# Kernel optimization log

Measured on AMD Instinct MI355X. Metric: run time of the kernel, lower is better.

Reference implementation:

```python
import math
import jax, jax.numpy as jnp
import numpy as np

B, T, C, H = 4, 2048, 1024, 16
D = C // H  # head dim = 64


def setup_inputs() -> dict:
    key = jax.random.key(0)
    ks = jax.random.split(key, 9)
    s = 1.0 / math.sqrt(C)
    return {
        "x": jax.random.normal(ks[0], (B, T, C), jnp.float32),
        "Wq": jax.random.normal(ks[1], (C, C), jnp.float32) * s,
        "bq": jax.random.normal(ks[2], (C,), jnp.float32) * 0.02,
        "Wk": jax.random.normal(ks[3], (C, C), jnp.float32) * s,
        "bk": jax.random.normal(ks[4], (C,), jnp.float32) * 0.02,
        "Wv": jax.random.normal(ks[5], (C, C), jnp.float32) * s,
        "bv": jax.random.normal(ks[6], (C,), jnp.float32) * 0.02,
        "Wo": jax.random.normal(ks[7], (C, C), jnp.float32) * s,
        "bo": jax.random.normal(ks[8], (C,), jnp.float32) * 0.02,
    }


def reference(x, Wq, bq, Wk, bk, Wv, bv, Wo, bo):
    # Projections: (B,T,C) -> (B,H,T,D)
    def heads(y):
        return y.reshape(B, T, H, D).transpose(0, 2, 1, 3)

    q = heads(x @ Wq + bq)
    k = heads(x @ Wk + bk)
    v = heads(x @ Wv + bv)

    scale = 1.0 / math.sqrt(D)
    scores = jnp.einsum("bhqd,bhkd->bhqk", q, k) * scale  # (B,H,T,T)
    causal = jnp.tril(jnp.ones((T, T), dtype=bool))
    scores = jnp.where(causal[None, None], scores, jnp.float32(-jnp.inf))
    att = jax.nn.softmax(scores, axis=-1)

    y = jnp.einsum("bhqk,bhkd->bhqd", att, v)  # (B,H,T,D)
    y = y.transpose(0, 2, 1, 3).reshape(B, T, C)
    return y @ Wo + bo
```

## Files before the change

### kernel.cpp

```cpp
#include <hip/hip_runtime.h>

#define B_ 4
#define T_ 2048
#define C_ 1024
#define H_ 16
#define D_ 64
#define M_ (B_*T_)

typedef unsigned short u16;
typedef __attribute__((ext_vector_type(8))) short short8;
typedef __attribute__((ext_vector_type(8))) unsigned short ushort8_t;
typedef __attribute__((ext_vector_type(4))) unsigned short ushort4_t;
typedef __attribute__((ext_vector_type(4))) float floatx4;
typedef __attribute__((ext_vector_type(16))) float f32x16;
typedef __attribute__((ext_vector_type(4))) unsigned int uint4_t;

__device__ __forceinline__ u16 f2bf(float f) {
  union { float f; unsigned u; } v; v.f = f;
  unsigned r = v.u + 0x7fffu + ((v.u >> 16) & 1u);
  return (u16)(r >> 16);
}

__device__ __forceinline__ void gload16(const void* g, void* l) {
  __builtin_amdgcn_global_load_lds((__attribute__((address_space(1))) void*)(g),
                                   (__attribute__((address_space(3))) void*)(l),
                                   16, 0, 0);
}

__device__ __forceinline__ unsigned cvtpk(float lo, float hi) {
  unsigned r;
  asm("v_cvt_pk_bf16_f32 %0, %1, %2" : "=v"(r) : "v"(lo), "v"(hi));
  return r;
}

__device__ __forceinline__ void pl32swap(unsigned &a, unsigned &b) {
  asm volatile("v_permlane32_swap_b32 %0, %1" : "+v"(a), "+v"(b));
}

__global__ __launch_bounds__(256) void convx_k(const float* __restrict__ x,
                                               u16* __restrict__ o) {
  int i = (blockIdx.x * 256 + threadIdx.x) * 4;
  floatx4 v = *(const floatx4*)(x + i);
  ushort4_t r;
#pragma unroll
  for (int j = 0; j < 4; ++j) r[j] = f2bf(v[j]);
  *(ushort4_t*)(o + i) = r;
}

__global__ __launch_bounds__(256) void wconv_k(const float* __restrict__ W0,
                                               const float* __restrict__ W1,
                                               const float* __restrict__ W2,
                                               const float* __restrict__ W3,
                                               u16* __restrict__ WT) {
  __shared__ float tile[64][65];
  const float* W = blockIdx.z == 0 ? W0 : blockIdx.z == 1 ? W1 : blockIdx.z == 2 ? W2 : W3;
  u16* Wt = WT + (size_t)blockIdx.z * (C_ * C_);
  int k0 = blockIdx.x * 64, n0 = blockIdx.y * 64;
  int t = threadIdx.x;
  int r = t >> 2, c0 = (t & 3) * 16;
#pragma unroll
  for (int j = 0; j < 4; ++j) {
    floatx4 v = *(const floatx4*)(W + (size_t)(k0 + r) * C_ + n0 + c0 + j * 4);
#pragma unroll
    for (int jj = 0; jj < 4; ++jj) tile[r][c0 + j * 4 + jj] = v[jj];
  }
  __syncthreads();
  ushort8_t o0, o1;
#pragma unroll
  for (int j = 0; j < 8; ++j) o0[j] = f2bf(tile[c0 + j][r]);
#pragma unroll
  for (int j = 0; j < 8; ++j) o1[j] = f2bf(tile[c0 + 8 + j][r]);
  *(ushort8_t*)(Wt + (size_t)(n0 + r) * C_ + k0 + c0) = o0;
  *(ushort8_t*)(Wt + (size_t)(n0 + r) * C_ + k0 + c0 + 8) = o1;
}

template <int OUTF32>
__global__ __launch_bounds__(256, 2) void gemm_k(const u16* __restrict__ A,
                                                 const u16* __restrict__ Wt,
                                                 const float* __restrict__ bias,
                                                 void* __restrict__ Cout, float scale) {
  __shared__ u16 As[128 * 32];
  __shared__ u16 Bs[128 * 32];
  const int tid = threadIdx.x;
  const int w = tid >> 6, lane = tid & 63;
  const int wr = (w >> 1) * 64, wc = (w & 1) * 64;
  const int l15 = lane & 15, g = lane >> 4;
  const int m0 = blockIdx.x * 128, n0 = blockIdx.y * 128;

  floatx4 acc[4][4] = {};

  const u16* ga = A + (size_t)(m0 + (tid >> 2)) * C_ + (tid & 3) * 8;
  const u16* gb = Wt + (size_t)(n0 + (tid >> 2)) * C_ + (tid & 3) * 8;
  u16* lA = As + tid * 8;
  u16* lB = Bs + tid * 8;

  for (int kt = 0; kt < C_; kt += 32) {
    gload16(ga + kt, lA);
    gload16(ga + kt + (size_t)64 * C_, lA + 64 * 32);
    gload16(gb + kt, lB);
    gload16(gb + kt + (size_t)64 * C_, lB + 64 * 32);
    asm volatile("s_waitcnt vmcnt(0)" ::: "memory");
    __syncthreads();
    short8 af[4], bf[4];
#pragma unroll
    for (int i = 0; i < 4; ++i)
      af[i] = *(const short8*)(As + (wr + i * 16 + l15) * 32 + g * 8);
#pragma unroll
    for (int i = 0; i < 4; ++i)
      bf[i] = *(const short8*)(Bs + (wc + i * 16 + l15) * 32 + g * 8);
#pragma unroll
    for (int mi = 0; mi < 4; ++mi)
#pragma unroll
      for (int ni = 0; ni < 4; ++ni)
        acc[mi][ni] = __builtin_amdgcn_mfma_f32_16x16x32_bf16(af[mi], bf[ni], acc[mi][ni], 0, 0, 0);
    __syncthreads();
  }
#pragma unroll
  for (int mi = 0; mi < 4; ++mi) {
    int row = m0 + wr + mi * 16 + g * 4;
#pragma unroll
    for (int ni = 0; ni < 4; ++ni) {
      int col = n0 + wc + ni * 16 + l15;
      float bv = bias[col];
#pragma unroll
      for (int i = 0; i < 4; ++i) {
        float v = (acc[mi][ni][i] + bv) * scale;
        if (OUTF32)
          ((float*)Cout)[(size_t)(row + i) * C_ + col] = v;
        else
          ((u16*)Cout)[(size_t)(row + i) * C_ + col] = f2bf(v);
      }
    }
  }
}

__global__ __launch_bounds__(512, 2) void attn_k(const u16* __restrict__ Qg,
                                                 const u16* __restrict__ Kg,
                                                 const u16* __restrict__ Vg,
                                                 u16* __restrict__ Yg) {
  __shared__ u16 Ks[2][64 * 64];
  __shared__ u16 Vt[2][64 * 64];

  const int tid = threadIdx.x;
  const int w = tid >> 6, lane = tid & 63;
  const int qi = lane & 31, h = lane >> 5;

  const int lid = blockIdx.x + 8 * blockIdx.y;
  const int xcd = lid & 7, slot = lid >> 3;
  const int bxl = 7 - (slot >> 3);
  const int bh = xcd + 8 * (slot & 7);
  const int q0 = bxl * 256;
  const size_t base = (size_t)(bh >> 4) * ((size_t)T_ * C_) + (size_t)(bh & 15) * D_;
  const int qw0 = q0 + w * 32;
  const int q_abs = qw0 + qi;

  const int srow = tid >> 3, schunk = tid & 7;
  const int sgcol = (schunk ^ (srow & 7)) * 8;
  const u16* Kgr = Kg + base + (size_t)srow * C_ + sgcol;
  const u16* Vgr = Vg + base + (size_t)srow * C_ + schunk * 8;

  short8 qf[4];
  {
    const u16* Qr = Qg + base + (size_t)q_abs * C_ + 8 * h;
#pragma unroll
    for (int c = 0; c < 4; ++c) qf[c] = *(const short8*)(Qr + 16 * c);
  }

  gload16(Kgr, &Ks[0][tid * 8]);
  ushort8_t va = *(const ushort8_t*)(Vgr);

  f32x16 y0 = {}, y1 = {};
  float m_run = -3e38f, l_run = 0.f;
  const int nt = 4 * bxl + 4;

  for (int t = 0; t < nt; ++t) {
    u16* Kb = Ks[t & 1];
    u16* Vb = Vt[t & 1];
    asm volatile("s_waitcnt vmcnt(0)" ::: "memory");
#pragma unroll
    for (int j = 0; j < 8; ++j) {
      int d = schunk * 8 + j;
      *(u16*)((char*)Vb + d * 128 + ((2 * srow) ^ (j << 4))) = va[j];
    }
    __syncthreads();
    if (t + 1 < nt) {
      gload16(Kgr + (size_t)(t + 1) * 64 * C_, &Ks[(t + 1) & 1][tid * 8]);
      va = *(const ushort8_t*)(Vgr + (size_t)(t + 1) * 64 * C_);
    }

    const int kv0 = t * 64;
    if (kv0 <= qw0 + 31) {
      f32x16 s0 = {}, s1 = {};
      {
        const char* kbase = (const char*)Kb;
        const int sw = (qi & 7) << 4;
        const char* kr0 = kbase + qi * 128;
        const char* kr1 = kbase + (qi + 32) * 128;
#pragma unroll
        for (int c = 0; c < 4; ++c) {
          int col = (32 * c + 16 * h) ^ sw;
          short8 k0 = *(const short8*)(kr0 + col);
          short8 k1 = *(const short8*)(kr1 + col);
          s0 = __builtin_amdgcn_mfma_f32_32x32x16_bf16(k0, qf[c], s0, 0, 0, 0);
          s1 = __builtin_amdgcn_mfma_f32_32x32x16_bf16(k1, qf[c], s1, 0, 0, 0);
        }
      }
      if (kv0 + 63 > qw0) {
#pragma unroll
        for (int r = 0; r < 16; ++r) {
          int kvq = (r & 3) + 8 * (r >> 2) + 4 * h;
          if (kv0 + kvq > q_abs) s0[r] = -1e30f;
          if (kv0 + 32 + kvq > q_abs) s1[r] = -1e30f;
        }
      }
      float pm = s0[0];
#pragma unroll
      for (int r = 1; r < 16; ++r) pm = fmaxf(pm, s0[r]);
#pragma unroll
      for (int r = 0; r < 16; ++r) pm = fmaxf(pm, s1[r]);
      pm = fmaxf(pm, __shfl_xor(pm, 32));
      if (!__all(pm <= m_run + 8.0f)) {
        float mnew = fmaxf(m_run, pm);
        float corr = __builtin_amdgcn_exp2f(m_run - mnew);
        m_run = mnew;
        l_run *= corr;
#pragma unroll
        for (int r = 0; r < 16; ++r) {
          float cq = __shfl(corr, (r & 3) + 8 * (r >> 2) + 4 * h);
          y0[r] *= cq;
          y1[r] *= cq;
        }
      }
      float rs = 0.f;
#pragma unroll
      for (int r = 0; r < 16; ++r) { s0[r] = __builtin_amdgcn_exp2f(s0[r] - m_run); rs += s0[r]; }
#pragma unroll
      for (int r = 0; r < 16; ++r) { s1[r] = __builtin_amdgcn_exp2f(s1[r] - m_run); rs += s1[r]; }
      rs += __shfl_xor(rs, 32);
      l_run += rs;

      float pv[32];
#pragma unroll
      for (int r = 0; r < 16; ++r) { pv[r] = s0[r]; pv[16 + r] = s1[r]; }
      unsigned pw[16];
#pragma unroll
      for (int c = 0; c < 4; ++c) {
        const int rb = c * 8;
        unsigned a0 = cvtpk(pv[rb + 0], pv[rb + 1]);
        unsigned b0 = cvtpk(pv[rb + 4], pv[rb + 5]);
        pl32swap(a0, b0);
        unsigned a1 = cvtpk(pv[rb + 2], pv[rb + 3]);
        unsigned b1 = cvtpk(pv[rb + 6], pv[rb + 7]);
        pl32swap(a1, b1);
        pw[c * 4 + 0] = a0; pw[c * 4 + 1] = a1;
        pw[c * 4 + 2] = b0; pw[c * 4 + 3] = b1;
      }
      {
        const char* vb0 = (const char*)Vb + qi * 128;
        const char* vb1 = (const char*)Vb + (qi + 32) * 128;
        const int swd = (qi & 7) << 4;
#pragma unroll
        for (int c = 0; c < 4; ++c) {
          int col = (32 * c + 16 * h) ^ swd;
          uint4_t pt = {pw[c * 4 + 0], pw[c * 4 + 1], pw[c * 4 + 2], pw[c * 4 + 3]};
          short8 pa = __builtin_bit_cast(short8, pt);
          short8 v0 = *(const short8*)(vb0 + col);
          short8 v1 = *(const short8*)(vb1 + col);
          y0 = __builtin_amdgcn_mfma_f32_32x32x16_bf16(pa, v0, y0, 0, 0, 0);
          y1 = __builtin_amdgcn_mfma_f32_32x32x16_bf16(pa, v1, y1, 0, 0, 0);
        }
      }
    }
    __syncthreads();
  }

  float linv = 1.0f / l_run;
#pragma unroll
  for (int r = 0; r < 16; ++r) {
    int qp = (r & 3) + 8 * (r >> 2) + 4 * h;
    float lv = __shfl(linv, qp);
    size_t row = base + (size_t)(qw0 + qp) * C_;
    Yg[row + qi] = f2bf(y0[r] * lv);
    Yg[row + 32 + qi] = f2bf(y1[r] * lv);
  }
}

extern "C" void kernel_launch(void* const* d_in, const int* in_sizes, int n_in,
                              void* d_out, int out_size, void* d_ws, size_t ws_size,
                              hipStream_t stream) {
  const float* x  = (const float*)d_in[0];
  const float* Wq = (const float*)d_in[1];
  const float* bq = (const float*)d_in[2];
  const float* Wk = (const float*)d_in[3];
  const float* bk = (const float*)d_in[4];
  const float* Wv = (const float*)d_in[5];
  const float* bv = (const float*)d_in[6];
  const float* Wo = (const float*)d_in[7];
  const float* bo = (const float*)d_in[8];
  float* out = (float*)d_out;

  char* ws = (char*)d_ws;
  u16* xb = (u16*)ws;
  u16* WT = (u16*)(ws + (size_t)16777216);
  u16* Qb = (u16*)(ws + (size_t)25165824);
  u16* Kb = (u16*)(ws + (size_t)41943040);
  u16* Vb = (u16*)(ws + (size_t)58720256);
  u16* Yb = xb;

  convx_k<<<dim3(M_ * C_ / 1024), 256, 0, stream>>>(x, xb);
  wconv_k<<<dim3(16, 16, 4), 256, 0, stream>>>(Wq, Wk, Wv, Wo, WT);
  gemm_k<0><<<dim3(64, 8), 256, 0, stream>>>(xb, WT + (size_t)0 * 1048576, bq, Qb, 0.125f * 1.44269504f);
  gemm_k<0><<<dim3(64, 8), 256, 0, stream>>>(xb, WT + (size_t)1 * 1048576, bk, Kb, 1.0f);
  gemm_k<0><<<dim3(64, 8), 256, 0, stream>>>(xb, WT + (size_t)2 * 1048576, bv, Vb, 1.0f);
  attn_k<<<dim3(8, 64), 512, 0, stream>>>(Qb, Kb, Vb, Yb);
  gemm_k<1><<<dim3(64, 8), 256, 0, stream>>>(Yb, WT + (size_t)3 * 1048576, bo, out, 1.0f);
}
```

Before: 197.7 us.

## Fuse QKV projections into one GEMM and pair causal query tiles in attention

Folds the softmax scale into the converted Wq weights and merges the three Q/K/V projection GEMMs into a single launch writing an interleaved QKV buffer with a 3072 stride. The attention kernel moves to 256-thread blocks with 1D indexing, and each block handles two 128-row query tiles (j and 15-j), so every block does the same amount of causal work. The goal is fewer launches, better wave fill in the projection, and less tail imbalance in attention. In exchange, Q is now scaled before rounding to bf16 rather than after, the epilogue picks a bias by segment, and the attention loop is longer and heavy on macros, with more live Q registers.

```diff
diff --git a/kernel.cpp b/kernel.cpp
--- a/kernel.cpp
+++ b/kernel.cpp
@@ -6,6 +6,7 @@
 #define H_ 16
 #define D_ 64
 #define M_ (B_*T_)
+#define CR3 3072
 
 typedef unsigned short u16;
 typedef __attribute__((ext_vector_type(8))) short short8;
@@ -37,6 +38,8 @@
   asm volatile("v_permlane32_swap_b32 %0, %1" : "+v"(a), "+v"(b));
 }
 
+#define MFMA32(a, b, c) __builtin_amdgcn_mfma_f32_32x32x16_bf16(a, b, c, 0, 0, 0)
+
 __global__ __launch_bounds__(256) void convx_k(const float* __restrict__ x,
                                                u16* __restrict__ o) {
   int i = (blockIdx.x * 256 + threadIdx.x) * 4;
@@ -54,6 +57,7 @@
                                                u16* __restrict__ WT) {
   __shared__ float tile[64][65];
   const float* W = blockIdx.z == 0 ? W0 : blockIdx.z == 1 ? W1 : blockIdx.z == 2 ? W2 : W3;
+  const float sc = blockIdx.z == 0 ? 0.125f * 1.44269504f : 1.0f;
   u16* Wt = WT + (size_t)blockIdx.z * (C_ * C_);
   int k0 = blockIdx.x * 64, n0 = blockIdx.y * 64;
   int t = threadIdx.x;
@@ -67,9 +71,9 @@
   __syncthreads();
   ushort8_t o0, o1;
 #pragma unroll
-  for (int j = 0; j < 8; ++j) o0[j] = f2bf(tile[c0 + j][r]);
-#pragma unroll
-  for (int j = 0; j < 8; ++j) o1[j] = f2bf(tile[c0 + 8 + j][r]);
+  for (int j = 0; j < 8; ++j) o0[j] = f2bf(tile[c0 + j][r] * sc);
+#pragma unroll
+  for (int j = 0; j < 8; ++j) o1[j] = f2bf(tile[c0 + 8 + j][r] * sc);
   *(ushort8_t*)(Wt + (size_t)(n0 + r) * C_ + k0 + c0) = o0;
   *(ushort8_t*)(Wt + (size_t)(n0 + r) * C_ + k0 + c0 + 8) = o1;
 }
@@ -77,8 +81,11 @@
 template <int OUTF32>
 __global__ __launch_bounds__(256, 2) void gemm_k(const u16* __restrict__ A,
                                                  const u16* __restrict__ Wt,
-                                                 const float* __restrict__ bias,
-                                                 void* __restrict__ Cout, float scale) {
+                                                 const float* __restrict__ b0,
+                                                 const float* __restrict__ b1,
+                                                 const float* __restrict__ b2,
+                                                 float bsc0,
+                                                 void* __restrict__ Cout, int ostride) {
   __shared__ u16 As[128 * 32];
   __shared__ u16 Bs[128 * 32];
   const int tid = threadIdx.x;
@@ -121,22 +128,22 @@
 #pragma unroll
     for (int ni = 0; ni < 4; ++ni) {
       int col = n0 + wc + ni * 16 + l15;
-      float bv = bias[col];
+      int seg = col >> 10;
+      const float* bp = seg == 0 ? b0 : seg == 1 ? b1 : b2;
+      float bv = bp[col & 1023] * (seg == 0 ? bsc0 : 1.0f);
 #pragma unroll
       for (int i = 0; i < 4; ++i) {
-        float v = (acc[mi][ni][i] + bv) * scale;
+        float v = acc[mi][ni][i] + bv;
         if (OUTF32)
-          ((float*)Cout)[(size_t)(row + i) * C_ + col] = v;
+          ((float*)Cout)[(size_t)(row + i) * ostride + col] = v;
         else
-          ((u16*)Cout)[(size_t)(row + i) * C_ + col] = f2bf(v);
+          ((u16*)Cout)[(size_t)(row + i) * ostride + col] = f2bf(v);
       }
     }
   }
 }
 
-__global__ __launch_bounds__(512, 2) void attn_k(const u16* __restrict__ Qg,
-                                                 const u16* __restrict__ Kg,
-                                                 const u16* __restrict__ Vg,
+__global__ __launch_bounds__(256, 2) void attn_k(const u16* __restrict__ QKV,
                                                  u16* __restrict__ Yg) {
   __shared__ u16 Ks[2][64 * 64];
   __shared__ u16 Vt[2][64 * 64];
@@ -145,143 +152,175 @@
   const int w = tid >> 6, lane = tid & 63;
   const int qi = lane & 31, h = lane >> 5;
 
-  const int lid = blockIdx.x + 8 * blockIdx.y;
-  const int xcd = lid & 7, slot = lid >> 3;
-  const int bxl = 7 - (slot >> 3);
-  const int bh = xcd + 8 * (slot & 7);
-  const int q0 = bxl * 256;
-  const size_t base = (size_t)(bh >> 4) * ((size_t)T_ * C_) + (size_t)(bh & 15) * D_;
-  const int qw0 = q0 + w * 32;
-  const int q_abs = qw0 + qi;
+  const int lid = blockIdx.x;
+  const int xcd = lid & 7, t2 = lid >> 3;
+  const int bh = xcd + 8 * (t2 & 7);
+  const int p = t2 >> 3;
+  const int jA = p, jB = 15 - p;
+  const int nA = 2 * jA + 2;
+
+  const size_t baseQ = (size_t)(bh >> 4) * T_ * CR3 + (size_t)(bh & 15) * D_;
+  const size_t baseY = (size_t)(bh >> 4) * T_ * C_ + (size_t)(bh & 15) * D_;
+  const u16* Kg = QKV + baseQ + 1024;
+  const u16* Vg = QKV + baseQ + 2048;
 
   const int srow = tid >> 3, schunk = tid & 7;
   const int sgcol = (schunk ^ (srow & 7)) * 8;
-  const u16* Kgr = Kg + base + (size_t)srow * C_ + sgcol;
-  const u16* Vgr = Vg + base + (size_t)srow * C_ + schunk * 8;
-
-  short8 qf[4];
+  const u16* Kgr = Kg + (size_t)srow * CR3 + sgcol;
+  const u16* Vgr = Vg + (size_t)srow * CR3 + schunk * 8;
+
+  short8 qA0, qA1, qA2, qA3, qB0, qB1, qB2, qB3;
   {
-    const u16* Qr = Qg + base + (size_t)q_abs * C_ + 8 * h;
-#pragma unroll
-    for (int c = 0; c < 4; ++c) qf[c] = *(const short8*)(Qr + 16 * c);
-  }
-
+    const u16* Qa = QKV + baseQ + (size_t)(128 * jA + 32 * w + qi) * CR3 + 8 * h;
+    const u16* Qb = QKV + baseQ + (size_t)(128 * jB + 32 * w + qi) * CR3 + 8 * h;
+    qA0 = *(const short8*)(Qa);      qA1 = *(const short8*)(Qa + 16);
+    qA2 = *(const short8*)(Qa + 32); qA3 = *(const short8*)(Qa + 48);
+    qB0 = *(const short8*)(Qb);      qB1 = *(const short8*)(Qb + 16);
+    qB2 = *(const short8*)(Qb + 32); qB3 = *(const short8*)(Qb + 48);
+  }
+
+  ushort8_t va, vbr;
   gload16(Kgr, &Ks[0][tid * 8]);
-  ushort8_t va = *(const ushort8_t*)(Vgr);
+  gload16(Kgr + (size_t)32 * CR3, &Ks[0][2048 + tid * 8]);
+  va = *(const ushort8_t*)(Vgr);
+  vbr = *(const ushort8_t*)(Vgr + (size_t)32 * CR3);
 
   f32x16 y0 = {}, y1 = {};
   float m_run = -3e38f, l_run = 0.f;
-  const int nt = 4 * bxl + 4;
-
-  for (int t = 0; t < nt; ++t) {
-    u16* Kb = Ks[t & 1];
-    u16* Vb = Vt[t & 1];
-    asm volatile("s_waitcnt vmcnt(0)" ::: "memory");
-#pragma unroll
-    for (int j = 0; j < 8; ++j) {
-      int d = schunk * 8 + j;
-      *(u16*)((char*)Vb + d * 128 + ((2 * srow) ^ (j << 4))) = va[j];
+
+#define PREFETCH(IT2) do { \
+    if ((IT2) < 34) { \
+      int nkv_ = ((IT2) >= nA ? (IT2) - nA : (IT2)) * 64; \
+      u16* dst_ = Ks[(IT2) & 1]; \
+      gload16(Kgr + (size_t)nkv_ * CR3, dst_ + tid * 8); \
+      gload16(Kgr + (size_t)(nkv_ + 32) * CR3, dst_ + 2048 + tid * 8); \
+      va = *(const ushort8_t*)(Vgr + (size_t)nkv_ * CR3); \
+      vbr = *(const ushort8_t*)(Vgr + (size_t)(nkv_ + 32) * CR3); \
+    } } while (0)
+
+#define SCATTERV(VB) do { \
+    char* vbp_ = (char*)(VB); \
+    _Pragma("unroll") for (int j = 0; j < 8; ++j) { \
+      int d_ = schunk * 8 + j; \
+      *(u16*)(vbp_ + d_ * 128 + ((2 * srow) ^ (j << 4))) = va[j]; \
+      *(u16*)(vbp_ + d_ * 128 + ((2 * (srow + 32)) ^ (j << 4))) = vbr[j]; \
+    } } while (0)
+
+#define COMPUTE(KB, VB, KV0, QW0, QF0, QF1, QF2, QF3) do { \
+    const int q_abs_ = (QW0) + qi; \
+    f32x16 s0 = {}, s1 = {}; \
+    { const int swq_ = (qi & 7) << 4; \
+      const char* kr0_ = (const char*)(KB) + qi * 128; \
+      const char* kr1_ = (const char*)(KB) + (qi + 32) * 128; \
+      short8 k0_, k1_; \
+      k0_ = *(const short8*)(kr0_ + ((16 * h) ^ swq_)); \
+      k1_ = *(const short8*)(kr1_ + ((16 * h) ^ swq_)); \
+      s0 = MFMA32(k0_, QF0, s0); s1 = MFMA32(k1_, QF0, s1); \
+      k0_ = *(const short8*)(kr0_ + ((32 + 16 * h) ^ swq_)); \
+      k1_ = *(const short8*)(kr1_ + ((32 + 16 * h) ^ swq_)); \
+      s0 = MFMA32(k0_, QF1, s0); s1 = MFMA32(k1_, QF1, s1); \
+      k0_ = *(const short8*)(kr0_ + ((64 + 16 * h) ^ swq_)); \
+      k1_ = *(const short8*)(kr1_ + ((64 + 16 * h) ^ swq_)); \
+      s0 = MFMA32(k0_, QF2, s0); s1 = MFMA32(k1_, QF2, s1); \
+      k0_ = *(const short8*)(kr0_ + ((96 + 16 * h) ^ swq_)); \
+      k1_ = *(const short8*)(kr1_ + ((96 + 16 * h) ^ swq_)); \
+      s0 = MFMA32(k0_, QF3, s0); s1 = MFMA32(k1_, QF3, s1); \
+    } \
+    if ((KV0) + 63 > (QW0)) { \
+      _Pragma("unroll") for (int r = 0; r < 16; ++r) { \
+        int kvq_ = (r & 3) + 8 * (r >> 2) + 4 * h; \
+        if ((KV0) + kvq_ > q_abs_) s0[r] = -1e30f; \
+        if ((KV0) + 32 + kvq_ > q_abs_) s1[r] = -1e30f; \
+      } \
+    } \
+    float pm_ = s0[0]; \
+    _Pragma("unroll") for (int r = 1; r < 16; ++r) pm_ = fmaxf(pm_, s0[r]); \
+    _Pragma("unroll") for (int r = 0; r < 16; ++r) pm_ = fmaxf(pm_, s1[r]); \
+    pm_ = fmaxf(pm_, __shfl_xor(pm_, 32)); \
+    if (!__all(pm_ <= m_run + 8.0f)) { \
+      float mnew_ = fmaxf(m_run, pm_); \
+      float corr_ = __builtin_amdgcn_exp2f(m_run - mnew_); \
+      m_run = mnew_; \
+      l_run *= corr_; \
+      _Pragma("unroll") for (int r = 0; r < 16; ++r) { \
+        float cq_ = __shfl(corr_, (r & 3) + 8 * (r >> 2) + 4 * h); \
+        y0[r] *= cq_; y1[r] *= cq_; \
+      } \
+    } \
+    float rs_ = 0.f; \
+    _Pragma("unroll") for (int r = 0; r < 16; ++r) { s0[r] = __builtin_amdgcn_exp2f(s0[r] - m_run); rs_ += s0[r]; } \
+    _Pragma("unroll") for (int r = 0; r < 16; ++r) { s1[r] = __builtin_amdgcn_exp2f(s1[r] - m_run); rs_ += s1[r]; } \
+    rs_ += __shfl_xor(rs_, 32); \
+    l_run += rs_; \
+    float pv_[32]; \
+    _Pragma("unroll") for (int r = 0; r < 16; ++r) { pv_[r] = s0[r]; pv_[16 + r] = s1[r]; } \
+    unsigned pw_[16]; \
+    _Pragma("unroll") for (int c = 0; c < 4; ++c) { \
+      const int rb_ = c * 8; \
+      unsigned a0_ = cvtpk(pv_[rb_ + 0], pv_[rb_ + 1]); \
+      unsigned b0_ = cvtpk(pv_[rb_ + 4], pv_[rb_ + 5]); \
+      pl32swap(a0_, b0_); \
+      unsigned a1_ = cvtpk(pv_[rb_ + 2], pv_[rb_ + 3]); \
+      unsigned b1_ = cvtpk(pv_[rb_ + 6], pv_[rb_ + 7]); \
+      pl32swap(a1_, b1_); \
+      pw_[c * 4 + 0] = a0_; pw_[c * 4 + 1] = a1_; \
+      pw_[c * 4 + 2] = b0_; pw_[c * 4 + 3] = b1_; \
+    } \
+    { const char* vb0_ = (const char*)(VB) + qi * 128; \
+      const char* vb1_ = (const char*)(VB) + (qi + 32) * 128; \
+      const int swd_ = (qi & 7) << 4; \
+      _Pragma("unroll") for (int c = 0; c < 4; ++c) { \
+        int col_ = (32 * c + 16 * h) ^ swd_; \
+        uint4_t pt_ = {pw_[c * 4 + 0], pw_[c * 4 + 1], pw_[c * 4 + 2], pw_[c * 4 + 3]}; \
+        short8 pa_ = __builtin_bit_cast(short8, pt_); \
+        short8 v0_ = *(const short8*)(vb0_ + col_); \
+        short8 v1_ = *(const short8*)(vb1_ + col_); \
+        y0 = MFMA32(pa_, v0_, y0); \
+        y1 = MFMA32(pa_, v1_, y1); \
+      } \
+    } } while (0)
+
+#define STOREY(J) do { \
+    float linv_ = 1.0f / l_run; \
+    _Pragma("unroll") for (int r = 0; r < 16; ++r) { \
+      int qp_ = (r & 3) + 8 * (r >> 2) + 4 * h; \
+      float lv_ = __shfl(linv_, qp_); \
+      size_t row_ = baseY + (size_t)(128 * (J) + 32 * w + qp_) * C_; \
+      Yg[row_ + qi] = f2bf(y0[r] * lv_); \
+      Yg[row_ + 32 + qi] = f2bf(y1[r] * lv_); \
+    } } while (0)
+
+  {
+    const int qw0 = 128 * jA + 32 * w;
+    for (int it = 0; it < nA; ++it) {
+      const int kv0 = it * 64;
+      u16* Kb = Ks[it & 1];
+      u16* Vb = Vt[it & 1];
+      asm volatile("s_waitcnt vmcnt(0)" ::: "memory");
+      SCATTERV(Vb);
+      __syncthreads();
+      PREFETCH(it + 1);
+      if (kv0 <= qw0 + 31) COMPUTE(Kb, Vb, kv0, qw0, qA0, qA1, qA2, qA3);
+      __syncthreads();
     }
-    __syncthreads();
-    if (t + 1 < nt) {
-      gload16(Kgr + (size_t)(t + 1) * 64 * C_, &Ks[(t + 1) & 1][tid * 8]);
-      va = *(const ushort8_t*)(Vgr + (size_t)(t + 1) * 64 * C_);
+    STOREY(jA);
+  }
+  y0 = (f32x16){}; y1 = (f32x16){};
+  m_run = -3e38f; l_run = 0.f;
+  {
+    const int qw0 = 128 * jB + 32 * w;
+    for (int it = nA; it < 34; ++it) {
+      const int kv0 = (it - nA) * 64;
+      u16* Kb = Ks[it & 1];
+      u16* Vb = Vt[it & 1];
+      asm volatile("s_waitcnt vmcnt(0)" ::: "memory");
+      SCATTERV(Vb);
+      __syncthreads();
+      PREFETCH(it + 1);
+      if (kv0 <= qw0 + 31) COMPUTE(Kb, Vb, kv0, qw0, qB0, qB1, qB2, qB3);
+      __syncthreads();
     }
-
-    const int kv0 = t * 64;
-    if (kv0 <= qw0 + 31) {
-      f32x16 s0 = {}, s1 = {};
-      {
-        const char* kbase = (const char*)Kb;
-        const int sw = (qi & 7) << 4;
-        const char* kr0 = kbase + qi * 128;
-        const char* kr1 = kbase + (qi + 32) * 128;
-#pragma unroll
-        for (int c = 0; c < 4; ++c) {
-          int col = (32 * c + 16 * h) ^ sw;
-          short8 k0 = *(const short8*)(kr0 + col);
-          short8 k1 = *(const short8*)(kr1 + col);
-          s0 = __builtin_amdgcn_mfma_f32_32x32x16_bf16(k0, qf[c], s0, 0, 0, 0);
-          s1 = __builtin_amdgcn_mfma_f32_32x32x16_bf16(k1, qf[c], s1, 0, 0, 0);
-        }
-      }
-      if (kv0 + 63 > qw0) {
-#pragma unroll
-        for (int r = 0; r < 16; ++r) {
-          int kvq = (r & 3) + 8 * (r >> 2) + 4 * h;
-          if (kv0 + kvq > q_abs) s0[r] = -1e30f;
-          if (kv0 + 32 + kvq > q_abs) s1[r] = -1e30f;
-        }
-      }
-      float pm = s0[0];
-#pragma unroll
-      for (int r = 1; r < 16; ++r) pm = fmaxf(pm, s0[r]);
-#pragma unroll
-      for (int r = 0; r < 16; ++r) pm = fmaxf(pm, s1[r]);
-      pm = fmaxf(pm, __shfl_xor(pm, 32));
-      if (!__all(pm <= m_run + 8.0f)) {
-        float mnew = fmaxf(m_run, pm);
-        float corr = __builtin_amdgcn_exp2f(m_run - mnew);
-        m_run = mnew;
-        l_run *= corr;
-#pragma unroll
-        for (int r = 0; r < 16; ++r) {
-          float cq = __shfl(corr, (r & 3) + 8 * (r >> 2) + 4 * h);
-          y0[r] *= cq;
-          y1[r] *= cq;
-        }
-      }
-      float rs = 0.f;
-#pragma unroll
-      for (int r = 0; r < 16; ++r) { s0[r] = __builtin_amdgcn_exp2f(s0[r] - m_run); rs += s0[r]; }
-#pragma unroll
-      for (int r = 0; r < 16; ++r) { s1[r] = __builtin_amdgcn_exp2f(s1[r] - m_run); rs += s1[r]; }
-      rs += __shfl_xor(rs, 32);
-      l_run += rs;
-
-      float pv[32];
-#pragma unroll
-      for (int r = 0; r < 16; ++r) { pv[r] = s0[r]; pv[16 + r] = s1[r]; }
-      unsigned pw[16];
-#pragma unroll
-      for (int c = 0; c < 4; ++c) {
-        const int rb = c * 8;
-        unsigned a0 = cvtpk(pv[rb + 0], pv[rb + 1]);
-        unsigned b0 = cvtpk(pv[rb + 4], pv[rb + 5]);
-        pl32swap(a0, b0);
-        unsigned a1 = cvtpk(pv[rb + 2], pv[rb + 3]);
-        unsigned b1 = cvtpk(pv[rb + 6], pv[rb + 7]);
-        pl32swap(a1, b1);
-        pw[c * 4 + 0] = a0; pw[c * 4 + 1] = a1;
-        pw[c * 4 + 2] = b0; pw[c * 4 + 3] = b1;
-      }
-      {
-        const char* vb0 = (const char*)Vb + qi * 128;
-        const char* vb1 = (const char*)Vb + (qi + 32) * 128;
-        const int swd = (qi & 7) << 4;
-#pragma unroll
-        for (int c = 0; c < 4; ++c) {
-          int col = (32 * c + 16 * h) ^ swd;
-          uint4_t pt = {pw[c * 4 + 0], pw[c * 4 + 1], pw[c * 4 + 2], pw[c * 4 + 3]};
-          short8 pa = __builtin_bit_cast(short8, pt);
-          short8 v0 = *(const short8*)(vb0 + col);
-          short8 v1 = *(const short8*)(vb1 + col);
-          y0 = __builtin_amdgcn_mfma_f32_32x32x16_bf16(pa, v0, y0, 0, 0, 0);
-          y1 = __builtin_amdgcn_mfma_f32_32x32x16_bf16(pa, v1, y1, 0, 0, 0);
-        }
-      }
-    }
-    __syncthreads();
-  }
-
-  float linv = 1.0f / l_run;
-#pragma unroll
-  for (int r = 0; r < 16; ++r) {
-    int qp = (r & 3) + 8 * (r >> 2) + 4 * h;
-    float lv = __shfl(linv, qp);
-    size_t row = base + (size_t)(qw0 + qp) * C_;
-    Yg[row + qi] = f2bf(y0[r] * lv);
-    Yg[row + 32 + qi] = f2bf(y1[r] * lv);
+    STOREY(jB);
   }
 }
 
@@ -300,18 +339,16 @@
   float* out = (float*)d_out;
 
   char* ws = (char*)d_ws;
-  u16* xb = (u16*)ws;
-  u16* WT = (u16*)(ws + (size_t)16777216);
-  u16* Qb = (u16*)(ws + (size_t)25165824);
-  u16* Kb = (u16*)(ws + (size_t)41943040);
-  u16* Vb = (u16*)(ws + (size_t)58720256);
+  u16* xb   = (u16*)ws;
+  u16* WT   = (u16*)(ws + (size_t)16777216);
+  u16* QKVb = (u16*)(ws + (size_t)25165824);
   u16* Yb = xb;
 
   convx_k<<<dim3(M_ * C_ / 1024), 256, 0, stream>>>(x, xb);
   wconv_k<<<dim3(16, 16, 4), 256, 0, stream>>>(Wq, Wk, Wv, Wo, WT);
-  gemm_k<0><<<dim3(64, 8), 256, 0, stream>>>(xb, WT + (size_t)0 * 1048576, bq, Qb, 0.125f * 1.44269504f);
-  gemm_k<0><<<dim3(64, 8), 256, 0, stream>>>(xb, WT + (size_t)1 * 1048576, bk, Kb, 1.0f);
-  gemm_k<0><<<dim3(64, 8), 256, 0, stream>>>(xb, WT + (size_t)2 * 1048576, bv, Vb, 1.0f);
-  attn_k<<<dim3(8, 64), 512, 0, stream>>>(Qb, Kb, Vb, Yb);
-  gemm_k<1><<<dim3(64, 8), 256, 0, stream>>>(Yb, WT + (size_t)3 * 1048576, bo, out, 1.0f);
-}
+  gemm_k<0><<<dim3(64, 24), 256, 0, stream>>>(xb, WT, bq, bk, bv, 0.125f * 1.44269504f,
+                                              QKVb, CR3);
+  attn_k<<<dim3(512), 256, 0, stream>>>(QKVb, Yb);
+  gemm_k<1><<<dim3(64, 8), 256, 0, stream>>>(Yb, WT + (size_t)3 * 1048576, bo, bo, bo, 1.0f,
+                                             out, C_);
+}
```

After: 190.4 us. -3.7%, faster.

## Fuse QKV projections into one GEMM and retile attention to 128-query blocks

Applied to the files above, without the earlier changes.

The three Q/K/V projection GEMMs become a single launch over a concatenated 3072-wide output. The Q scale is folded into the converted Wq weights and the bias is picked per column segment. Attention now reads the interleaved QKV buffer with 256-thread blocks covering 128 query rows, scheduled in a balanced causal order, and uses a new V-transpose swizzle. This cuts launch overhead, improves wave fill and load balance, and lowers LDS bank conflicts, at the cost of strided QKV reads and more K/V tile reloads per query.

```diff
diff --git a/kernel.cpp b/kernel.cpp
--- a/kernel.cpp
+++ b/kernel.cpp
@@ -6,6 +6,7 @@
 #define H_ 16
 #define D_ 64
 #define M_ (B_*T_)
+#define CR3 3072
 
 typedef unsigned short u16;
 typedef __attribute__((ext_vector_type(8))) short short8;
@@ -37,6 +38,8 @@
   asm volatile("v_permlane32_swap_b32 %0, %1" : "+v"(a), "+v"(b));
 }
 
+#define MFMA32(a, b, c) __builtin_amdgcn_mfma_f32_32x32x16_bf16(a, b, c, 0, 0, 0)
+
 __global__ __launch_bounds__(256) void convx_k(const float* __restrict__ x,
                                                u16* __restrict__ o) {
   int i = (blockIdx.x * 256 + threadIdx.x) * 4;
@@ -54,6 +57,7 @@
                                                u16* __restrict__ WT) {
   __shared__ float tile[64][65];
   const float* W = blockIdx.z == 0 ? W0 : blockIdx.z == 1 ? W1 : blockIdx.z == 2 ? W2 : W3;
+  const float sc = blockIdx.z == 0 ? 0.125f * 1.44269504f : 1.0f;
   u16* Wt = WT + (size_t)blockIdx.z * (C_ * C_);
   int k0 = blockIdx.x * 64, n0 = blockIdx.y * 64;
   int t = threadIdx.x;
@@ -67,9 +71,9 @@
   __syncthreads();
   ushort8_t o0, o1;
 #pragma unroll
-  for (int j = 0; j < 8; ++j) o0[j] = f2bf(tile[c0 + j][r]);
-#pragma unroll
-  for (int j = 0; j < 8; ++j) o1[j] = f2bf(tile[c0 + 8 + j][r]);
+  for (int j = 0; j < 8; ++j) o0[j] = f2bf(tile[c0 + j][r] * sc);
+#pragma unroll
+  for (int j = 0; j < 8; ++j) o1[j] = f2bf(tile[c0 + 8 + j][r] * sc);
   *(ushort8_t*)(Wt + (size_t)(n0 + r) * C_ + k0 + c0) = o0;
   *(ushort8_t*)(Wt + (size_t)(n0 + r) * C_ + k0 + c0 + 8) = o1;
 }
@@ -77,8 +81,11 @@
 template <int OUTF32>
 __global__ __launch_bounds__(256, 2) void gemm_k(const u16* __restrict__ A,
                                                  const u16* __restrict__ Wt,
-                                                 const float* __restrict__ bias,
-                                                 void* __restrict__ Cout, float scale) {
+                                                 const float* __restrict__ b0,
+                                                 const float* __restrict__ b1,
+                                                 const float* __restrict__ b2,
+                                                 float bsc0,
+                                                 void* __restrict__ Cout, int ostride) {
   __shared__ u16 As[128 * 32];
   __shared__ u16 Bs[128 * 32];
   const int tid = threadIdx.x;
@@ -121,22 +128,22 @@
 #pragma unroll
     for (int ni = 0; ni < 4; ++ni) {
       int col = n0 + wc + ni * 16 + l15;
-      float bv = bias[col];
+      int seg = col >> 10;
+      const float* bp = seg == 0 ? b0 : seg == 1 ? b1 : b2;
+      float bv = bp[col & 1023] * (seg == 0 ? bsc0 : 1.0f);
 #pragma unroll
       for (int i = 0; i < 4; ++i) {
-        float v = (acc[mi][ni][i] + bv) * scale;
+        float v = acc[mi][ni][i] + bv;
         if (OUTF32)
-          ((float*)Cout)[(size_t)(row + i) * C_ + col] = v;
+          ((float*)Cout)[(size_t)(row + i) * ostride + col] = v;
         else
-          ((u16*)Cout)[(size_t)(row + i) * C_ + col] = f2bf(v);
+          ((u16*)Cout)[(size_t)(row + i) * ostride + col] = f2bf(v);
       }
     }
   }
 }
 
-__global__ __launch_bounds__(512, 2) void attn_k(const u16* __restrict__ Qg,
-                                                 const u16* __restrict__ Kg,
-                                                 const u16* __restrict__ Vg,
+__global__ __launch_bounds__(256, 4) void attn_k(const u16* __restrict__ QKV,
                                                  u16* __restrict__ Yg) {
   __shared__ u16 Ks[2][64 * 64];
   __shared__ u16 Vt[2][64 * 64];
@@ -145,65 +152,86 @@
   const int w = tid >> 6, lane = tid & 63;
   const int qi = lane & 31, h = lane >> 5;
 
-  const int lid = blockIdx.x + 8 * blockIdx.y;
-  const int xcd = lid & 7, slot = lid >> 3;
-  const int bxl = 7 - (slot >> 3);
-  const int bh = xcd + 8 * (slot & 7);
-  const int q0 = bxl * 256;
-  const size_t base = (size_t)(bh >> 4) * ((size_t)T_ * C_) + (size_t)(bh & 15) * D_;
-  const int qw0 = q0 + w * 32;
-  const int q_abs = qw0 + qi;
+  const int lid = blockIdx.x;
+  const int a4 = lid >> 6;
+  const int gq = a4 >> 2, iq = a4 & 3;
+  const int jt = gq == 0 ? 15 - 2 * iq : gq == 1 ? 2 * iq : gq == 2 ? 14 - 2 * iq : 1 + 2 * iq;
+  const int bh = lid & 63;
+  const int nt = 2 * jt + 2;
+
+  const size_t baseQ = (size_t)(bh >> 4) * T_ * CR3 + (size_t)(bh & 15) * D_;
+  const size_t baseY = (size_t)(bh >> 4) * T_ * C_ + (size_t)(bh & 15) * D_;
+  const u16* Kg = QKV + baseQ + 1024;
+  const u16* Vg = QKV + baseQ + 2048;
 
   const int srow = tid >> 3, schunk = tid & 7;
   const int sgcol = (schunk ^ (srow & 7)) * 8;
-  const u16* Kgr = Kg + base + (size_t)srow * C_ + sgcol;
-  const u16* Vgr = Vg + base + (size_t)srow * C_ + schunk * 8;
-
-  short8 qf[4];
+  const u16* Kgr = Kg + (size_t)srow * CR3 + sgcol;
+  const u16* Vgr = Vg + (size_t)srow * CR3 + schunk * 8;
+
+  const int qw0 = 128 * jt + 32 * w;
+  const int q_abs = qw0 + qi;
+
+  short8 qf0, qf1, qf2, qf3;
   {
-    const u16* Qr = Qg + base + (size_t)q_abs * C_ + 8 * h;
-#pragma unroll
-    for (int c = 0; c < 4; ++c) qf[c] = *(const short8*)(Qr + 16 * c);
-  }
-
+    const u16* Qr = QKV + baseQ + (size_t)q_abs * CR3 + 8 * h;
+    qf0 = *(const short8*)(Qr);      qf1 = *(const short8*)(Qr + 16);
+    qf2 = *(const short8*)(Qr + 32); qf3 = *(const short8*)(Qr + 48);
+  }
+
+  ushort8_t va, vbr;
   gload16(Kgr, &Ks[0][tid * 8]);
-  ushort8_t va = *(const ushort8_t*)(Vgr);
+  gload16(Kgr + (size_t)32 * CR3, &Ks[0][2048 + tid * 8]);
+  va = *(const ushort8_t*)(Vgr);
+  vbr = *(const ushort8_t*)(Vgr + (size_t)32 * CR3);
 
   f32x16 y0 = {}, y1 = {};
   float m_run = -3e38f, l_run = 0.f;
-  const int nt = 4 * bxl + 4;
 
   for (int t = 0; t < nt; ++t) {
+    const int kv0 = t * 64;
     u16* Kb = Ks[t & 1];
     u16* Vb = Vt[t & 1];
     asm volatile("s_waitcnt vmcnt(0)" ::: "memory");
-#pragma unroll
-    for (int j = 0; j < 8; ++j) {
-      int d = schunk * 8 + j;
-      *(u16*)((char*)Vb + d * 128 + ((2 * srow) ^ (j << 4))) = va[j];
+    {
+      char* vbp = (char*)Vb;
+#pragma unroll
+      for (int j = 0; j < 8; ++j) {
+        int d = schunk * 8 + j;
+        int sl = ((schunk ^ j) & 7) << 4;
+        *(u16*)(vbp + d * 128 + ((2 * srow) ^ sl)) = va[j];
+        *(u16*)(vbp + d * 128 + ((2 * (srow + 32)) ^ sl)) = vbr[j];
+      }
     }
     __syncthreads();
     if (t + 1 < nt) {
-      gload16(Kgr + (size_t)(t + 1) * 64 * C_, &Ks[(t + 1) & 1][tid * 8]);
-      va = *(const ushort8_t*)(Vgr + (size_t)(t + 1) * 64 * C_);
+      int nkv = (t + 1) * 64;
+      u16* dst = Ks[(t + 1) & 1];
+      gload16(Kgr + (size_t)nkv * CR3, dst + tid * 8);
+      gload16(Kgr + (size_t)(nkv + 32) * CR3, dst + 2048 + tid * 8);
+      va = *(const ushort8_t*)(Vgr + (size_t)nkv * CR3);
+      vbr = *(const ushort8_t*)(Vgr + (size_t)(nkv + 32) * CR3);
     }
 
-    const int kv0 = t * 64;
     if (kv0 <= qw0 + 31) {
       f32x16 s0 = {}, s1 = {};
       {
-        const char* kbase = (const char*)Kb;
-        const int sw = (qi & 7) << 4;
-        const char* kr0 = kbase + qi * 128;
-        const char* kr1 = kbase + (qi + 32) * 128;
-#pragma unroll
-        for (int c = 0; c < 4; ++c) {
-          int col = (32 * c + 16 * h) ^ sw;
-          short8 k0 = *(const short8*)(kr0 + col);
-          short8 k1 = *(const short8*)(kr1 + col);
-          s0 = __builtin_amdgcn_mfma_f32_32x32x16_bf16(k0, qf[c], s0, 0, 0, 0);
-          s1 = __builtin_amdgcn_mfma_f32_32x32x16_bf16(k1, qf[c], s1, 0, 0, 0);
-        }
+        const int swq = (qi & 7) << 4;
+        const char* kr0 = (const char*)Kb + qi * 128;
+        const char* kr1 = (const char*)Kb + (qi + 32) * 128;
+        short8 k0, k1;
+        k0 = *(const short8*)(kr0 + ((16 * h) ^ swq));
+        k1 = *(const short8*)(kr1 + ((16 * h) ^ swq));
+        s0 = MFMA32(k0, qf0, s0); s1 = MFMA32(k1, qf0, s1);
+        k0 = *(const short8*)(kr0 + ((32 + 16 * h) ^ swq));
+        k1 = *(const short8*)(kr1 + ((32 + 16 * h) ^ swq));
+        s0 = MFMA32(k0, qf1, s0); s1 = MFMA32(k1, qf1, s1);
+        k0 = *(const short8*)(kr0 + ((64 + 16 * h) ^ swq));
+        k1 = *(const short8*)(kr1 + ((64 + 16 * h) ^ swq));
+        s0 = MFMA32(k0, qf2, s0); s1 = MFMA32(k1, qf2, s1);
+        k0 = *(const short8*)(kr0 + ((96 + 16 * h) ^ swq));
+        k1 = *(const short8*)(kr1 + ((96 + 16 * h) ^ swq));
+        s0 = MFMA32(k0, qf3, s0); s1 = MFMA32(k1, qf3, s1);
       }
       if (kv0 + 63 > qw0) {
 #pragma unroll
@@ -258,16 +286,17 @@
       {
         const char* vb0 = (const char*)Vb + qi * 128;
         const char* vb1 = (const char*)Vb + (qi + 32) * 128;
-        const int swd = (qi & 7) << 4;
+        const int sx0 = (((qi >> 3) ^ qi) & 7) << 4;
+        const int sx1 = sx0 ^ 0x40;
 #pragma unroll
         for (int c = 0; c < 4; ++c) {
-          int col = (32 * c + 16 * h) ^ swd;
+          int cb = 32 * c + 16 * h;
           uint4_t pt = {pw[c * 4 + 0], pw[c * 4 + 1], pw[c * 4 + 2], pw[c * 4 + 3]};
           short8 pa = __builtin_bit_cast(short8, pt);
-          short8 v0 = *(const short8*)(vb0 + col);
-          short8 v1 = *(const short8*)(vb1 + col);
-          y0 = __builtin_amdgcn_mfma_f32_32x32x16_bf16(pa, v0, y0, 0, 0, 0);
-          y1 = __builtin_amdgcn_mfma_f32_32x32x16_bf16(pa, v1, y1, 0, 0, 0);
+          short8 v0 = *(const short8*)(vb0 + (cb ^ sx0));
+          short8 v1 = *(const short8*)(vb1 + (cb ^ sx1));
+          y0 = MFMA32(pa, v0, y0);
+          y1 = MFMA32(pa, v1, y1);
         }
       }
     }
@@ -279,7 +308,7 @@
   for (int r = 0; r < 16; ++r) {
     int qp = (r & 3) + 8 * (r >> 2) + 4 * h;
     float lv = __shfl(linv, qp);
-    size_t row = base + (size_t)(qw0 + qp) * C_;
+    size_t row = baseY + (size_t)(qw0 + qp) * C_;
     Yg[row + qi] = f2bf(y0[r] * lv);
     Yg[row + 32 + qi] = f2bf(y1[r] * lv);
   }
@@ -300,18 +329,16 @@
   float* out = (float*)d_out;
 
   char* ws = (char*)d_ws;
-  u16* xb = (u16*)ws;
-  u16* WT = (u16*)(ws + (size_t)16777216);
-  u16* Qb = (u16*)(ws + (size_t)25165824);
-  u16* Kb = (u16*)(ws + (size_t)41943040);
-  u16* Vb = (u16*)(ws + (size_t)58720256);
+  u16* xb   = (u16*)ws;
+  u16* WT   = (u16*)(ws + (size_t)16777216);
+  u16* QKVb = (u16*)(ws + (size_t)25165824);
   u16* Yb = xb;
 
   convx_k<<<dim3(M_ * C_ / 1024), 256, 0, stream>>>(x, xb);
   wconv_k<<<dim3(16, 16, 4), 256, 0, stream>>>(Wq, Wk, Wv, Wo, WT);
-  gemm_k<0><<<dim3(64, 8), 256, 0, stream>>>(xb, WT + (size_t)0 * 1048576, bq, Qb, 0.125f * 1.44269504f);
-  gemm_k<0><<<dim3(64, 8), 256, 0, stream>>>(xb, WT + (size_t)1 * 1048576, bk, Kb, 1.0f);
-  gemm_k<0><<<dim3(64, 8), 256, 0, stream>>>(xb, WT + (size_t)2 * 1048576, bv, Vb, 1.0f);
-  attn_k<<<dim3(8, 64), 512, 0, stream>>>(Qb, Kb, Vb, Yb);
-  gemm_k<1><<<dim3(64, 8), 256, 0, stream>>>(Yb, WT + (size_t)3 * 1048576, bo, out, 1.0f);
-}
+  gemm_k<0><<<dim3(64, 24), 256, 0, stream>>>(xb, WT, bq, bk, bv, 0.125f * 1.44269504f,
+                                              QKVb, CR3);
+  attn_k<<<dim3(1024), 256, 0, stream>>>(QKVb, Yb);
+  gemm_k<1><<<dim3(64, 8), 256, 0, stream>>>(Yb, WT + (size_t)3 * 1048576, bo, bo, bo, 1.0f,
+                                             out, C_);
+}
```

Result: faster. 184.6 us (-6.6%).
